# Performance work log

Measured on AMD Instinct MI355X. Metric: run time of the kernel, lower is better.

The kernel has to match this reference:

```python
import jax, jax.numpy as jnp
import numpy as np

N_NODES = 100_000
N_EDGES = 1_600_000
F_NODE = 128
F_EDGE = 128
HIDDEN = 256
OUT = 128


def setup_inputs() -> dict:
    key = jax.random.key(0)
    k = jax.random.split(key, 7)
    x = jax.random.normal(k[0], (N_NODES, F_NODE), dtype=jnp.float32)
    edge_index = jax.random.randint(k[1], (2, N_EDGES), 0, N_NODES, dtype=jnp.int64)
    edge_attr = jax.random.normal(k[2], (N_EDGES, F_EDGE), dtype=jnp.float32)
    fan_in1 = F_NODE + F_EDGE
    W1 = jax.random.normal(k[3], (HIDDEN, fan_in1), dtype=jnp.float32) / np.sqrt(fan_in1)
    b1 = jnp.zeros((HIDDEN,), dtype=jnp.float32)
    W2 = jax.random.normal(k[4], (OUT, HIDDEN), dtype=jnp.float32) / np.sqrt(HIDDEN)
    b2 = jnp.zeros((OUT,), dtype=jnp.float32)
    return {"x": x, "edge_index": edge_index, "edge_attr": edge_attr,
            "W1": W1, "b1": b1, "W2": W2, "b2": b2}


def reference(x, edge_index, edge_attr, W1, b1, W2, b2):
    col = edge_index[1]
    # scatter-mean of edge_attr into target nodes (dim_size = #nodes)
    summed = jax.ops.segment_sum(edge_attr, col, num_segments=N_NODES)  # [N, F_edge]
    counts = jax.ops.segment_sum(jnp.ones((edge_attr.shape[0],), dtype=edge_attr.dtype),
                                 col, num_segments=N_NODES)
    agg = summed / jnp.maximum(counts, 1.0)[:, None]
    h = jnp.concatenate([x, agg], axis=1)          # [N, F_node + F_edge]
    h = jax.nn.relu(h @ W1.T + b1)                 # hidden Linear + ReLU
    return h @ W2.T + b2                           # final linear layer
```

## Files before the change

### kernel.cpp

```cpp
#include <hip/hip_runtime.h>
#include <hip/hip_bf16.h>
#include <stdint.h>

#define N_NODES 100000
#define N_EDGES 1600000
#define F_NODE 128
#define F_EDGE 128
#define HIDDEN 256
#define OUT_F 128
#define K_DIM 256
#define CAP 64

#define FILL_BLOCKS ((N_EDGES + 255) / 256)
#define CVT_BLOCKS  ((HIDDEN * K_DIM + OUT_F * HIDDEN) / 4 / 256)

using f32x4 = __attribute__((ext_vector_type(4))) float;
using s16x8 = __attribute__((ext_vector_type(8))) short;

typedef __attribute__((address_space(3))) unsigned lds_u32;
typedef __attribute__((address_space(1))) const unsigned gbl_u32;

static __device__ __forceinline__ short f2b(float f) {
  union { float f; unsigned u; } v; v.f = f;
  unsigned r = v.u + 0x7fffu + ((v.u >> 16) & 1u);
  return (short)(r >> 16);
}
static __device__ __forceinline__ void gld_lds16(const void* g, void* l) {
  __builtin_amdgcn_global_load_lds((gbl_u32*)g, (lds_u32*)l, 16, 0, 0);
}


__global__ void k_fill_cvt(const int* __restrict__ col,
                           unsigned* __restrict__ cursor,
                           unsigned* __restrict__ ids,
                           const float* __restrict__ W1,
                           const float* __restrict__ W2,
                           short* __restrict__ w1b,
                           short* __restrict__ w2b) {
  int bid = blockIdx.x;
  if (bid < FILL_BLOCKS) {
    int e = bid * 256 + threadIdx.x;
    if (e < N_EDGES) {
      int n = col[e];
      unsigned slot = atomicAdd(&cursor[n], 1u);
      if (slot < CAP) ids[(size_t)n * CAP + slot] = (unsigned)e;
    }
  } else {
    int i = ((bid - FILL_BLOCKS) * 256 + threadIdx.x) * 4;
    if (i < HIDDEN * K_DIM) {
      f32x4 v = *reinterpret_cast<const f32x4*>(W1 + i);
      short4 s; s.x = f2b(v[0]); s.y = f2b(v[1]); s.z = f2b(v[2]); s.w = f2b(v[3]);
      *reinterpret_cast<short4*>(w1b + i) = s;
    } else {
      int j = i - HIDDEN * K_DIM;
      if (j < OUT_F * HIDDEN) {
        f32x4 v = *reinterpret_cast<const f32x4*>(W2 + j);
        short4 s; s.x = f2b(v[0]); s.y = f2b(v[1]); s.z = f2b(v[2]); s.w = f2b(v[3]);
        *reinterpret_cast<short4*>(w2b + j) = s;
      }
    }
  }
}


__global__ __launch_bounds__(256, 8) void k_agg(const float* __restrict__ x,
                                                const float* __restrict__ edge_attr,
                                                const unsigned* __restrict__ cursor,
                                                const unsigned* __restrict__ ids,
                                                short* __restrict__ hin) {
  int n = (int)((blockIdx.x * (unsigned)blockDim.x + threadIdx.x) >> 6);
  int lane = threadIdx.x & 63;
  if (n >= N_NODES) return;
  int half = lane >> 5, l32 = lane & 31;
  unsigned cnt = cursor[n]; cnt = cnt > CAP ? CAP : cnt;
  const unsigned* idp = ids + (size_t)n * CAP;
  f32x4 a = {0.f, 0.f, 0.f, 0.f};
  const float* eb = edge_attr + 4 * l32;
  unsigned i = 0;
  for (; i + 8 <= cnt; i += 8) {
    unsigned e0 = idp[i + 0 + half];
    unsigned e1 = idp[i + 2 + half];
    unsigned e2 = idp[i + 4 + half];
    unsigned e3 = idp[i + 6 + half];
    f32x4 v0 = *reinterpret_cast<const f32x4*>(eb + (size_t)e0 * F_EDGE);
    f32x4 v1 = *reinterpret_cast<const f32x4*>(eb + (size_t)e1 * F_EDGE);
    f32x4 v2 = *reinterpret_cast<const f32x4*>(eb + (size_t)e2 * F_EDGE);
    f32x4 v3 = *reinterpret_cast<const f32x4*>(eb + (size_t)e3 * F_EDGE);
    a += (v0 + v1) + (v2 + v3);
  }
  for (; i + 2 <= cnt; i += 2) {
    unsigned e = idp[i + half];
    a += *reinterpret_cast<const f32x4*>(eb + (size_t)e * F_EDGE);
  }
  if (i < cnt && half == 0) {
    unsigned e = idp[i];
    a += *reinterpret_cast<const f32x4*>(eb + (size_t)e * F_EDGE);
  }
  f32x4 bsw;
  bsw[0] = __shfl_xor(a[0], 32); bsw[1] = __shfl_xor(a[1], 32);
  bsw[2] = __shfl_xor(a[2], 32); bsw[3] = __shfl_xor(a[3], 32);
  a += bsw;
  float inv = 1.0f / (float)(cnt > 0u ? cnt : 1u);
  float2 xv = *reinterpret_cast<const float2*>(x + (size_t)n * F_NODE + 2 * lane);
  short2 hx; hx.x = f2b(xv.x); hx.y = f2b(xv.y);
  short* hrow = hin + (size_t)n * K_DIM;
  *reinterpret_cast<short2*>(hrow + 2 * lane) = hx;
  if (half == 0) {
    short4 hm;
    hm.x = f2b(a[0] * inv); hm.y = f2b(a[1] * inv);
    hm.z = f2b(a[2] * inv); hm.w = f2b(a[3] * inv);
    *reinterpret_cast<short4*>(hrow + F_NODE + 4 * l32) = hm;
  }
}


__global__ __launch_bounds__(256) void k_mlp(const short* __restrict__ A,
                                             const short* __restrict__ W1b,
                                             const float* __restrict__ b1,
                                             const short* __restrict__ W2b,
                                             const float* __restrict__ b2,
                                             float* __restrict__ out, int M) {
  __shared__ short lds[64 * 256];
  const int t = threadIdx.x;
  const int lane = t & 63, wid = t >> 6;
  const int mrow0 = blockIdx.x * 64;
  const int lr = lane & 15;
  const int lkb = (lane >> 4) << 4;
  char* ldsb = (char*)lds;

#pragma unroll
  for (int j = 0; j < 8; ++j) {
    int chunk = j * 256 + t;
    int row = chunk >> 5;
    int kb = (chunk & 31) << 4;
    int src_kb = kb ^ ((row & 15) << 5);
    int grow = mrow0 + row; grow = grow < M ? grow : M - 1;
    const char* gsrc = (const char*)A + (size_t)grow * 512 + src_kb;
    char* ldst = ldsb + (size_t)(j * 256 + wid * 64) * 16;
    gld_lds16(gsrc, ldst);
  }
  __syncthreads();

  const int wc = wid;
  f32x4 acc1[4][4] = {};
  for (int ksb = 0; ksb < 512; ksb += 64) {
    s16x8 af[4], bf[4];
#pragma unroll
    for (int m = 0; m < 4; ++m) {
      int row = m * 16 + lr;
      int kb = (ksb + lkb) ^ ((row & 15) << 5);
      af[m] = *reinterpret_cast<const s16x8*>(ldsb + row * 512 + kb);
    }
#pragma unroll
    for (int nn = 0; nn < 4; ++nn) {
      int c = wc * 64 + nn * 16 + lr;
      bf[nn] = *reinterpret_cast<const s16x8*>(W1b + (size_t)c * 256 + ((ksb + lkb) >> 1));
    }
#pragma unroll
    for (int m = 0; m < 4; ++m)
#pragma unroll
      for (int nn = 0; nn < 4; ++nn)
        acc1[m][nn] = __builtin_amdgcn_mfma_f32_16x16x32_bf16(af[m], bf[nn], acc1[m][nn], 0, 0, 0);
  }
  __syncthreads();

#pragma unroll
  for (int nn = 0; nn < 4; ++nn) {
    int c = wc * 64 + nn * 16 + lr;
    float bv = b1[c];
#pragma unroll
    for (int m = 0; m < 4; ++m) {
#pragma unroll
      for (int j = 0; j < 4; ++j) {
        int r = m * 16 + (lane >> 4) * 4 + j;
        float v = acc1[m][nn][j] + bv;
        v = v > 0.f ? v : 0.f;
        *reinterpret_cast<short*>(ldsb + r * 512 + ((c * 2) ^ ((r & 15) << 5))) = f2b(v);
      }
    }
  }
  __syncthreads();

  const int wr2 = wid >> 1;
  const int wc2 = wid & 1;
  f32x4 acc2[2][4] = {};
  for (int ksb = 0; ksb < 512; ksb += 64) {
    s16x8 af[2], bf[4];
#pragma unroll
    for (int m = 0; m < 2; ++m) {
      int row = wr2 * 32 + m * 16 + lr;
      int kb = (ksb + lkb) ^ ((row & 15) << 5);
      af[m] = *reinterpret_cast<const s16x8*>(ldsb + row * 512 + kb);
    }
#pragma unroll
    for (int nn = 0; nn < 4; ++nn) {
      int c = wc2 * 64 + nn * 16 + lr;
      bf[nn] = *reinterpret_cast<const s16x8*>(W2b + (size_t)c * 256 + ((ksb + lkb) >> 1));
    }
#pragma unroll
    for (int m = 0; m < 2; ++m)
#pragma unroll
      for (int nn = 0; nn < 4; ++nn)
        acc2[m][nn] = __builtin_amdgcn_mfma_f32_16x16x32_bf16(af[m], bf[nn], acc2[m][nn], 0, 0, 0);
  }
#pragma unroll
  for (int nn = 0; nn < 4; ++nn) {
    int c = wc2 * 64 + nn * 16 + lr;
    float bv = b2[c];
#pragma unroll
    for (int m = 0; m < 2; ++m) {
#pragma unroll
      for (int j = 0; j < 4; ++j) {
        int r = mrow0 + wr2 * 32 + m * 16 + (lane >> 4) * 4 + j;
        if (r < M) out[(size_t)r * OUT_F + c] = acc2[m][nn][j] + bv;
      }
    }
  }
}


extern "C" void kernel_launch(void* const* d_in, const int* in_sizes, int n_in,
                              void* d_out, int out_size, void* d_ws, size_t ws_size,
                              hipStream_t stream) {
  const float* x         = (const float*)d_in[0];
  const int*   edge_idx  = (const int*)d_in[1];
  const int*   col       = edge_idx + N_EDGES;
  const float* edge_attr = (const float*)d_in[2];
  const float* W1        = (const float*)d_in[3];
  const float* b1        = (const float*)d_in[4];
  const float* W2        = (const float*)d_in[5];
  const float* b2        = (const float*)d_in[6];
  float* out = (float*)d_out;

  char* ws = (char*)d_ws;
  unsigned* cursor = (unsigned*)(ws + 0);
  unsigned* ids    = (unsigned*)(ws + 400000);
  short*    hin    = (short*)   (ws + 26000000);
  short*    w1b    = (short*)   (ws + 77200000);
  short*    w2b    = (short*)   (ws + 77331072);

  hipMemsetAsync(cursor, 0, 400000, stream);

  k_fill_cvt<<<FILL_BLOCKS + CVT_BLOCKS, 256, 0, stream>>>(col, cursor, ids,
                                                           W1, W2, w1b, w2b);
  k_agg<<<(N_NODES * 64 + 255) / 256, 256, 0, stream>>>(x, edge_attr, cursor, ids, hin);
  k_mlp<<<(N_NODES + 63) / 64, 256, 0, stream>>>(hin, w1b, b1, w2b, b2, out, N_NODES);
}
```

Before: 411.8 us.

## Replace capped index gather with counting-sort scatter of bf16 edge rows

Builds per-node CSR offsets via a count pass and a wave-scan with atomic bases, then scatters each edge_attr row (converted to bf16) into contiguous per-node buckets. The aggregation kernel then streams contiguous bf16 rows instead of gathering random fp32 rows through an index list. This aims to turn random reads into coalesced streams and halve the re-read bytes, but adds an extra 400MB scattered write plus its read-back, more atomics, two more launches, and bf16 rounding before summation. It also drops the 64-edge-per-node cap.

```diff
diff --git a/kernel.cpp b/kernel.cpp
--- a/kernel.cpp
+++ b/kernel.cpp
@@ -9,10 +9,9 @@
 #define HIDDEN 256
 #define OUT_F 128
 #define K_DIM 256
-#define CAP 64
-
-#define FILL_BLOCKS ((N_EDGES + 255) / 256)
-#define CVT_BLOCKS  ((HIDDEN * K_DIM + OUT_F * HIDDEN) / 4 / 256)
+
+#define COUNT_BLOCKS ((N_EDGES + 255) / 256)
+#define CVT_BLOCKS   ((HIDDEN * K_DIM + OUT_F * HIDDEN) / 4 / 256)
 
 using f32x4 = __attribute__((ext_vector_type(4))) float;
 using s16x8 = __attribute__((ext_vector_type(8))) short;
@@ -25,28 +24,27 @@
   unsigned r = v.u + 0x7fffu + ((v.u >> 16) & 1u);
   return (short)(r >> 16);
 }
+static __device__ __forceinline__ float b2f(unsigned short h) {
+  union { unsigned u; float f; } v; v.u = ((unsigned)h) << 16;
+  return v.f;
+}
 static __device__ __forceinline__ void gld_lds16(const void* g, void* l) {
   __builtin_amdgcn_global_load_lds((gbl_u32*)g, (lds_u32*)l, 16, 0, 0);
 }
 
 
-__global__ void k_fill_cvt(const int* __restrict__ col,
-                           unsigned* __restrict__ cursor,
-                           unsigned* __restrict__ ids,
-                           const float* __restrict__ W1,
-                           const float* __restrict__ W2,
-                           short* __restrict__ w1b,
-                           short* __restrict__ w2b) {
+__global__ void k_count_cvt(const int* __restrict__ col,
+                            unsigned* __restrict__ counts,
+                            const float* __restrict__ W1,
+                            const float* __restrict__ W2,
+                            short* __restrict__ w1b,
+                            short* __restrict__ w2b) {
   int bid = blockIdx.x;
-  if (bid < FILL_BLOCKS) {
+  if (bid < COUNT_BLOCKS) {
     int e = bid * 256 + threadIdx.x;
-    if (e < N_EDGES) {
-      int n = col[e];
-      unsigned slot = atomicAdd(&cursor[n], 1u);
-      if (slot < CAP) ids[(size_t)n * CAP + slot] = (unsigned)e;
-    }
+    if (e < N_EDGES) atomicAdd(&counts[col[e]], 1u);
   } else {
-    int i = ((bid - FILL_BLOCKS) * 256 + threadIdx.x) * 4;
+    int i = ((bid - COUNT_BLOCKS) * 256 + threadIdx.x) * 4;
     if (i < HIDDEN * K_DIM) {
       f32x4 v = *reinterpret_cast<const f32x4*>(W1 + i);
       short4 s; s.x = f2b(v[0]); s.y = f2b(v[1]); s.z = f2b(v[2]); s.w = f2b(v[3]);
@@ -63,54 +61,109 @@
 }
 
 
-__global__ __launch_bounds__(256, 8) void k_agg(const float* __restrict__ x,
-                                                const float* __restrict__ edge_attr,
-                                                const unsigned* __restrict__ cursor,
-                                                const unsigned* __restrict__ ids,
-                                                short* __restrict__ hin) {
+__global__ void k_offsets(const unsigned* __restrict__ counts,
+                          unsigned* __restrict__ offsets,
+                          unsigned* __restrict__ cursor,
+                          unsigned* __restrict__ total) {
+  int n = blockIdx.x * blockDim.x + threadIdx.x;
+  int lane = threadIdx.x & 63;
+  unsigned c = (n < N_NODES) ? counts[n] : 0u;
+  unsigned s = c;
+#pragma unroll
+  for (int d = 1; d < 64; d <<= 1) {
+    unsigned t = __shfl_up(s, d, 64);
+    if (lane >= d) s += t;
+  }
+  unsigned wave_sum = __shfl(s, 63, 64);
+  unsigned base = 0;
+  if (lane == 63) base = atomicAdd(total, wave_sum);
+  base = __shfl(base, 63, 64);
+  if (n < N_NODES) {
+    unsigned o = base + s - c;
+    offsets[n] = o;
+    cursor[n] = o;
+  }
+}
+
+
+__global__ __launch_bounds__(256) void k_scatter(const int* __restrict__ col,
+                                                 const float* __restrict__ edge_attr,
+                                                 unsigned* __restrict__ cursor,
+                                                 unsigned short* __restrict__ buckets) {
+  int h = (int)((blockIdx.x * (unsigned)blockDim.x + threadIdx.x) >> 5);
+  int l32 = threadIdx.x & 31;
+  int half = (threadIdx.x >> 5) & 1;
+  size_t ebase = (size_t)h * 4;
+  if (ebase >= N_EDGES) return;
+
+  unsigned slot = 0;
+  if (l32 < 4) {
+    int n = col[ebase + l32];
+    slot = atomicAdd(&cursor[n], 1u);
+  }
+  const float* eb = edge_attr + 4 * l32;
+  f32x4 v0 = *reinterpret_cast<const f32x4*>(eb + (ebase + 0) * F_EDGE);
+  f32x4 v1 = *reinterpret_cast<const f32x4*>(eb + (ebase + 1) * F_EDGE);
+  f32x4 v2 = *reinterpret_cast<const f32x4*>(eb + (ebase + 2) * F_EDGE);
+  f32x4 v3 = *reinterpret_cast<const f32x4*>(eb + (ebase + 3) * F_EDGE);
+  unsigned d0 = __shfl(slot, half * 32 + 0, 64);
+  unsigned d1 = __shfl(slot, half * 32 + 1, 64);
+  unsigned d2 = __shfl(slot, half * 32 + 2, 64);
+  unsigned d3 = __shfl(slot, half * 32 + 3, 64);
+  short4 s0, s1, s2, s3;
+  s0.x = f2b(v0[0]); s0.y = f2b(v0[1]); s0.z = f2b(v0[2]); s0.w = f2b(v0[3]);
+  s1.x = f2b(v1[0]); s1.y = f2b(v1[1]); s1.z = f2b(v1[2]); s1.w = f2b(v1[3]);
+  s2.x = f2b(v2[0]); s2.y = f2b(v2[1]); s2.z = f2b(v2[2]); s2.w = f2b(v2[3]);
+  s3.x = f2b(v3[0]); s3.y = f2b(v3[1]); s3.z = f2b(v3[2]); s3.w = f2b(v3[3]);
+  *reinterpret_cast<short4*>(buckets + (size_t)d0 * F_EDGE + 4 * l32) = s0;
+  *reinterpret_cast<short4*>(buckets + (size_t)d1 * F_EDGE + 4 * l32) = s1;
+  *reinterpret_cast<short4*>(buckets + (size_t)d2 * F_EDGE + 4 * l32) = s2;
+  *reinterpret_cast<short4*>(buckets + (size_t)d3 * F_EDGE + 4 * l32) = s3;
+}
+
+
+__global__ __launch_bounds__(256, 8) void k_agg2(const float* __restrict__ x,
+                                                 const unsigned* __restrict__ counts,
+                                                 const unsigned* __restrict__ offsets,
+                                                 const unsigned short* __restrict__ buckets,
+                                                 short* __restrict__ hin) {
   int n = (int)((blockIdx.x * (unsigned)blockDim.x + threadIdx.x) >> 6);
   int lane = threadIdx.x & 63;
   if (n >= N_NODES) return;
-  int half = lane >> 5, l32 = lane & 31;
-  unsigned cnt = cursor[n]; cnt = cnt > CAP ? CAP : cnt;
-  const unsigned* idp = ids + (size_t)n * CAP;
-  f32x4 a = {0.f, 0.f, 0.f, 0.f};
-  const float* eb = edge_attr + 4 * l32;
+  unsigned cnt = counts[n], off = offsets[n];
+  const unsigned short* bp = buckets + (size_t)off * F_EDGE + 2 * lane;
+  float a0 = 0.f, a1 = 0.f;
   unsigned i = 0;
   for (; i + 8 <= cnt; i += 8) {
-    unsigned e0 = idp[i + 0 + half];
-    unsigned e1 = idp[i + 2 + half];
-    unsigned e2 = idp[i + 4 + half];
-    unsigned e3 = idp[i + 6 + half];
-    f32x4 v0 = *reinterpret_cast<const f32x4*>(eb + (size_t)e0 * F_EDGE);
-    f32x4 v1 = *reinterpret_cast<const f32x4*>(eb + (size_t)e1 * F_EDGE);
-    f32x4 v2 = *reinterpret_cast<const f32x4*>(eb + (size_t)e2 * F_EDGE);
-    f32x4 v3 = *reinterpret_cast<const f32x4*>(eb + (size_t)e3 * F_EDGE);
-    a += (v0 + v1) + (v2 + v3);
-  }
-  for (; i + 2 <= cnt; i += 2) {
-    unsigned e = idp[i + half];
-    a += *reinterpret_cast<const f32x4*>(eb + (size_t)e * F_EDGE);
-  }
-  if (i < cnt && half == 0) {
-    unsigned e = idp[i];
-    a += *reinterpret_cast<const f32x4*>(eb + (size_t)e * F_EDGE);
-  }
-  f32x4 bsw;
-  bsw[0] = __shfl_xor(a[0], 32); bsw[1] = __shfl_xor(a[1], 32);
-  bsw[2] = __shfl_xor(a[2], 32); bsw[3] = __shfl_xor(a[3], 32);
-  a += bsw;
+    unsigned r0 = *reinterpret_cast<const unsigned*>(bp + (size_t)(i + 0) * F_EDGE);
+    unsigned r1 = *reinterpret_cast<const unsigned*>(bp + (size_t)(i + 1) * F_EDGE);
+    unsigned r2 = *reinterpret_cast<const unsigned*>(bp + (size_t)(i + 2) * F_EDGE);
+    unsigned r3 = *reinterpret_cast<const unsigned*>(bp + (size_t)(i + 3) * F_EDGE);
+    unsigned r4 = *reinterpret_cast<const unsigned*>(bp + (size_t)(i + 4) * F_EDGE);
+    unsigned r5 = *reinterpret_cast<const unsigned*>(bp + (size_t)(i + 5) * F_EDGE);
+    unsigned r6 = *reinterpret_cast<const unsigned*>(bp + (size_t)(i + 6) * F_EDGE);
+    unsigned r7 = *reinterpret_cast<const unsigned*>(bp + (size_t)(i + 7) * F_EDGE);
+    a0 += b2f((unsigned short)(r0 & 0xffffu)) + b2f((unsigned short)(r1 & 0xffffu))
+        + b2f((unsigned short)(r2 & 0xffffu)) + b2f((unsigned short)(r3 & 0xffffu))
+        + b2f((unsigned short)(r4 & 0xffffu)) + b2f((unsigned short)(r5 & 0xffffu))
+        + b2f((unsigned short)(r6 & 0xffffu)) + b2f((unsigned short)(r7 & 0xffffu));
+    a1 += b2f((unsigned short)(r0 >> 16)) + b2f((unsigned short)(r1 >> 16))
+        + b2f((unsigned short)(r2 >> 16)) + b2f((unsigned short)(r3 >> 16))
+        + b2f((unsigned short)(r4 >> 16)) + b2f((unsigned short)(r5 >> 16))
+        + b2f((unsigned short)(r6 >> 16)) + b2f((unsigned short)(r7 >> 16));
+  }
+  for (; i < cnt; ++i) {
+    unsigned r = *reinterpret_cast<const unsigned*>(bp + (size_t)i * F_EDGE);
+    a0 += b2f((unsigned short)(r & 0xffffu));
+    a1 += b2f((unsigned short)(r >> 16));
+  }
   float inv = 1.0f / (float)(cnt > 0u ? cnt : 1u);
   float2 xv = *reinterpret_cast<const float2*>(x + (size_t)n * F_NODE + 2 * lane);
   short2 hx; hx.x = f2b(xv.x); hx.y = f2b(xv.y);
+  short2 hm; hm.x = f2b(a0 * inv); hm.y = f2b(a1 * inv);
   short* hrow = hin + (size_t)n * K_DIM;
   *reinterpret_cast<short2*>(hrow + 2 * lane) = hx;
-  if (half == 0) {
-    short4 hm;
-    hm.x = f2b(a[0] * inv); hm.y = f2b(a[1] * inv);
-    hm.z = f2b(a[2] * inv); hm.w = f2b(a[3] * inv);
-    *reinterpret_cast<short4*>(hrow + F_NODE + 4 * l32) = hm;
-  }
+  *reinterpret_cast<short2*>(hrow + F_NODE + 2 * lane) = hm;
 }
 
 
@@ -233,16 +286,20 @@
   float* out = (float*)d_out;
 
   char* ws = (char*)d_ws;
-  unsigned* cursor = (unsigned*)(ws + 0);
-  unsigned* ids    = (unsigned*)(ws + 400000);
-  short*    hin    = (short*)   (ws + 26000000);
-  short*    w1b    = (short*)   (ws + 77200000);
-  short*    w2b    = (short*)   (ws + 77331072);
-
-  hipMemsetAsync(cursor, 0, 400000, stream);
-
-  k_fill_cvt<<<FILL_BLOCKS + CVT_BLOCKS, 256, 0, stream>>>(col, cursor, ids,
-                                                           W1, W2, w1b, w2b);
-  k_agg<<<(N_NODES * 64 + 255) / 256, 256, 0, stream>>>(x, edge_attr, cursor, ids, hin);
-  k_mlp<<<(N_NODES + 63) / 64, 256, 0, stream>>>(hin, w1b, b1, w2b, b2, out, N_NODES);
-}
+  unsigned*       counts  = (unsigned*)      (ws + 0);
+  unsigned*       total   = (unsigned*)      (ws + 400000);
+  unsigned*       offsets = (unsigned*)      (ws + 400016);
+  unsigned*       cursor  = (unsigned*)      (ws + 800016);
+  unsigned short* buckets = (unsigned short*)(ws + 1200032);
+  short*          hin     = (short*)         (ws + 410800032);
+  short*          w1b     = (short*)         (ws + 462000032);
+  short*          w2b     = (short*)         (ws + 462131104);
+
+  hipMemsetAsync(ws, 0, 400016, stream);
+
+  k_count_cvt<<<COUNT_BLOCKS + CVT_BLOCKS, 256, 0, stream>>>(col, counts, W1, W2, w1b, w2b);
+  k_offsets  <<<(N_NODES + 255) / 256, 256, 0, stream>>>(counts, offsets, cursor, total);
+  k_scatter  <<<N_EDGES / 4 * 32 / 256, 256, 0, stream>>>(col, edge_attr, cursor, buckets);
+  k_agg2     <<<(N_NODES * 64 + 255) / 256, 256, 0, stream>>>(x, counts, offsets, buckets, hin);
+  k_mlp      <<<(N_NODES + 63) / 64, 256, 0, stream>>>(hin, w1b, b1, w2b, b2, out, N_NODES);
+}
```

New measurement: 628.0 us. +52.5%, slower.

## Bucket edges into 48-node partitions and sort per partition in LDS

Applied to the files above, without the earlier changes.

Edges are no longer appended to per-node 64-slot lists with 100k atomic counters. They go into per-partition queues (48 nodes per partition, 1024 slots each) that pack the local node id and edge id into one word. Each reduce block then counting-sorts its partition queue in shared memory and gathers edge_attr per node from there. This shrinks the memset and the index buffer and spreads the atomics over fewer, coarser counters. In exchange, atomic contention on the 2084 counters goes up, the block does an extra in-LDS sort pass, and a partition whose edges exceed 1024 is silently truncated.

```diff
diff --git a/kernel.cpp b/kernel.cpp
--- a/kernel.cpp
+++ b/kernel.cpp
@@ -9,10 +9,13 @@
 #define HIDDEN 256
 #define OUT_F 128
 #define K_DIM 256
-#define CAP 64
-
-#define FILL_BLOCKS ((N_EDGES + 255) / 256)
-#define CVT_BLOCKS  ((HIDDEN * K_DIM + OUT_F * HIDDEN) / 4 / 256)
+
+#define PN 48
+#define NPART 2084
+#define QCAP 1024
+
+#define COUNT_BLOCKS ((N_EDGES + 255) / 256)
+#define CVT_BLOCKS   ((HIDDEN * K_DIM + OUT_F * HIDDEN) / 4 / 256)
 
 using f32x4 = __attribute__((ext_vector_type(4))) float;
 using s16x8 = __attribute__((ext_vector_type(8))) short;
@@ -30,23 +33,25 @@
 }
 
 
-__global__ void k_fill_cvt(const int* __restrict__ col,
-                           unsigned* __restrict__ cursor,
-                           unsigned* __restrict__ ids,
-                           const float* __restrict__ W1,
-                           const float* __restrict__ W2,
-                           short* __restrict__ w1b,
-                           short* __restrict__ w2b) {
+__global__ void k_scatter_cvt(const int* __restrict__ col,
+                              unsigned* __restrict__ qcur,
+                              unsigned* __restrict__ queue,
+                              const float* __restrict__ W1,
+                              const float* __restrict__ W2,
+                              short* __restrict__ w1b,
+                              short* __restrict__ w2b) {
   int bid = blockIdx.x;
-  if (bid < FILL_BLOCKS) {
+  if (bid < COUNT_BLOCKS) {
     int e = bid * 256 + threadIdx.x;
     if (e < N_EDGES) {
-      int n = col[e];
-      unsigned slot = atomicAdd(&cursor[n], 1u);
-      if (slot < CAP) ids[(size_t)n * CAP + slot] = (unsigned)e;
+      unsigned n = (unsigned)col[e];
+      unsigned p = n / PN;
+      unsigned nl = n - p * PN;
+      unsigned slot = atomicAdd(&qcur[p], 1u);
+      if (slot < QCAP) queue[(size_t)p * QCAP + slot] = (nl << 21) | (unsigned)e;
     }
   } else {
-    int i = ((bid - FILL_BLOCKS) * 256 + threadIdx.x) * 4;
+    int i = ((bid - COUNT_BLOCKS) * 256 + threadIdx.x) * 4;
     if (i < HIDDEN * K_DIM) {
       f32x4 v = *reinterpret_cast<const f32x4*>(W1 + i);
       short4 s; s.x = f2b(v[0]); s.y = f2b(v[1]); s.z = f2b(v[2]); s.w = f2b(v[3]);
@@ -63,53 +68,89 @@
 }
 
 
-__global__ __launch_bounds__(256, 8) void k_agg(const float* __restrict__ x,
-                                                const float* __restrict__ edge_attr,
-                                                const unsigned* __restrict__ cursor,
-                                                const unsigned* __restrict__ ids,
-                                                short* __restrict__ hin) {
-  int n = (int)((blockIdx.x * (unsigned)blockDim.x + threadIdx.x) >> 6);
-  int lane = threadIdx.x & 63;
-  if (n >= N_NODES) return;
+__global__ __launch_bounds__(256, 8) void k_reduce(const float* __restrict__ x,
+                                                   const float* __restrict__ edge_attr,
+                                                   const unsigned* __restrict__ qcur,
+                                                   const unsigned* __restrict__ queue,
+                                                   short* __restrict__ hin) {
+  __shared__ unsigned cnt48[PN];
+  __shared__ unsigned cur48[PN];
+  __shared__ unsigned sorted[QCAP];
+  int p = blockIdx.x;
+  int t = threadIdx.x;
+  if (t < PN) cnt48[t] = 0u;
+  __syncthreads();
+
+  unsigned qn = qcur[p]; if (qn > QCAP) qn = QCAP;
+  const unsigned* q = queue + (size_t)p * QCAP;
+  for (unsigned i = t; i < qn; i += 256)
+    atomicAdd(&cnt48[q[i] >> 21], 1u);
+  __syncthreads();
+
+  if (t < 64) {
+    unsigned c = (t < PN) ? cnt48[t] : 0u;
+    unsigned s = c;
+#pragma unroll
+    for (int d = 1; d < 64; d <<= 1) {
+      unsigned u = __shfl_up(s, d, 64);
+      if (t >= d) s += u;
+    }
+    if (t < PN) cur48[t] = s - c;
+  }
+  __syncthreads();
+
+  for (unsigned i = t; i < qn; i += 256) {
+    unsigned rec = q[i];
+    unsigned slot = atomicAdd(&cur48[rec >> 21], 1u);
+    sorted[slot] = rec & 0x1FFFFFu;
+  }
+  __syncthreads();
+
+  int lane = t & 63, wv = t >> 6;
   int half = lane >> 5, l32 = lane & 31;
-  unsigned cnt = cursor[n]; cnt = cnt > CAP ? CAP : cnt;
-  const unsigned* idp = ids + (size_t)n * CAP;
-  f32x4 a = {0.f, 0.f, 0.f, 0.f};
   const float* eb = edge_attr + 4 * l32;
-  unsigned i = 0;
-  for (; i + 8 <= cnt; i += 8) {
-    unsigned e0 = idp[i + 0 + half];
-    unsigned e1 = idp[i + 2 + half];
-    unsigned e2 = idp[i + 4 + half];
-    unsigned e3 = idp[i + 6 + half];
-    f32x4 v0 = *reinterpret_cast<const f32x4*>(eb + (size_t)e0 * F_EDGE);
-    f32x4 v1 = *reinterpret_cast<const f32x4*>(eb + (size_t)e1 * F_EDGE);
-    f32x4 v2 = *reinterpret_cast<const f32x4*>(eb + (size_t)e2 * F_EDGE);
-    f32x4 v3 = *reinterpret_cast<const f32x4*>(eb + (size_t)e3 * F_EDGE);
-    a += (v0 + v1) + (v2 + v3);
-  }
-  for (; i + 2 <= cnt; i += 2) {
-    unsigned e = idp[i + half];
-    a += *reinterpret_cast<const f32x4*>(eb + (size_t)e * F_EDGE);
-  }
-  if (i < cnt && half == 0) {
-    unsigned e = idp[i];
-    a += *reinterpret_cast<const f32x4*>(eb + (size_t)e * F_EDGE);
-  }
-  f32x4 bsw;
-  bsw[0] = __shfl_xor(a[0], 32); bsw[1] = __shfl_xor(a[1], 32);
-  bsw[2] = __shfl_xor(a[2], 32); bsw[3] = __shfl_xor(a[3], 32);
-  a += bsw;
-  float inv = 1.0f / (float)(cnt > 0u ? cnt : 1u);
-  float2 xv = *reinterpret_cast<const float2*>(x + (size_t)n * F_NODE + 2 * lane);
-  short2 hx; hx.x = f2b(xv.x); hx.y = f2b(xv.y);
-  short* hrow = hin + (size_t)n * K_DIM;
-  *reinterpret_cast<short2*>(hrow + 2 * lane) = hx;
-  if (half == 0) {
-    short4 hm;
-    hm.x = f2b(a[0] * inv); hm.y = f2b(a[1] * inv);
-    hm.z = f2b(a[2] * inv); hm.w = f2b(a[3] * inv);
-    *reinterpret_cast<short4*>(hrow + F_NODE + 4 * l32) = hm;
+  for (int k = 0; k < PN / 4; ++k) {
+    int nl = wv * (PN / 4) + k;
+    int gn = p * PN + nl;
+    if (gn >= N_NODES) break;
+    unsigned cnt = cnt48[nl];
+    unsigned base = cur48[nl] - cnt;
+    f32x4 a = {0.f, 0.f, 0.f, 0.f};
+    unsigned i = 0;
+    for (; i + 8 <= cnt; i += 8) {
+      unsigned e0 = sorted[base + i + 0 + half];
+      unsigned e1 = sorted[base + i + 2 + half];
+      unsigned e2 = sorted[base + i + 4 + half];
+      unsigned e3 = sorted[base + i + 6 + half];
+      f32x4 v0 = *reinterpret_cast<const f32x4*>(eb + (size_t)e0 * F_EDGE);
+      f32x4 v1 = *reinterpret_cast<const f32x4*>(eb + (size_t)e1 * F_EDGE);
+      f32x4 v2 = *reinterpret_cast<const f32x4*>(eb + (size_t)e2 * F_EDGE);
+      f32x4 v3 = *reinterpret_cast<const f32x4*>(eb + (size_t)e3 * F_EDGE);
+      a += (v0 + v1) + (v2 + v3);
+    }
+    for (; i + 2 <= cnt; i += 2) {
+      unsigned e = sorted[base + i + half];
+      a += *reinterpret_cast<const f32x4*>(eb + (size_t)e * F_EDGE);
+    }
+    if (i < cnt && half == 0) {
+      unsigned e = sorted[base + i];
+      a += *reinterpret_cast<const f32x4*>(eb + (size_t)e * F_EDGE);
+    }
+    f32x4 bsw;
+    bsw[0] = __shfl_xor(a[0], 32); bsw[1] = __shfl_xor(a[1], 32);
+    bsw[2] = __shfl_xor(a[2], 32); bsw[3] = __shfl_xor(a[3], 32);
+    a += bsw;
+    float inv = 1.0f / (float)(cnt > 0u ? cnt : 1u);
+    float2 xv = *reinterpret_cast<const float2*>(x + (size_t)gn * F_NODE + 2 * lane);
+    short2 hx; hx.x = f2b(xv.x); hx.y = f2b(xv.y);
+    short* hrow = hin + (size_t)gn * K_DIM;
+    *reinterpret_cast<short2*>(hrow + 2 * lane) = hx;
+    if (half == 0) {
+      short4 hm;
+      hm.x = f2b(a[0] * inv); hm.y = f2b(a[1] * inv);
+      hm.z = f2b(a[2] * inv); hm.w = f2b(a[3] * inv);
+      *reinterpret_cast<short4*>(hrow + F_NODE + 4 * l32) = hm;
+    }
   }
 }
 
@@ -233,16 +274,16 @@
   float* out = (float*)d_out;
 
   char* ws = (char*)d_ws;
-  unsigned* cursor = (unsigned*)(ws + 0);
-  unsigned* ids    = (unsigned*)(ws + 400000);
-  short*    hin    = (short*)   (ws + 26000000);
-  short*    w1b    = (short*)   (ws + 77200000);
-  short*    w2b    = (short*)   (ws + 77331072);
-
-  hipMemsetAsync(cursor, 0, 400000, stream);
-
-  k_fill_cvt<<<FILL_BLOCKS + CVT_BLOCKS, 256, 0, stream>>>(col, cursor, ids,
-                                                           W1, W2, w1b, w2b);
-  k_agg<<<(N_NODES * 64 + 255) / 256, 256, 0, stream>>>(x, edge_attr, cursor, ids, hin);
-  k_mlp<<<(N_NODES + 63) / 64, 256, 0, stream>>>(hin, w1b, b1, w2b, b2, out, N_NODES);
-}
+  unsigned* qcur  = (unsigned*)(ws + 0);
+  unsigned* queue = (unsigned*)(ws + 8352);
+  short*    hin   = (short*)   (ws + 8544416);
+  short*    w1b   = (short*)   (ws + 59744416);
+  short*    w2b   = (short*)   (ws + 59875488);
+
+  hipMemsetAsync(qcur, 0, NPART * 4, stream);
+
+  k_scatter_cvt<<<COUNT_BLOCKS + CVT_BLOCKS, 256, 0, stream>>>(col, qcur, queue,
+                                                               W1, W2, w1b, w2b);
+  k_reduce<<<NPART, 256, 0, stream>>>(x, edge_attr, qcur, queue, hin);
+  k_mlp   <<<(N_NODES + 63) / 64, 256, 0, stream>>>(hin, w1b, b1, w2b, b2, out, N_NODES);
+}
```

After: 503.7 us. 22.3% more time.
